# Kernel optimization log

Measured on AMD Instinct MI355X. Metric: run time of the kernel, lower is better.

## Reference

```python
import jax, jax.numpy as jnp
import numpy as np
import math

B, L, D_IN = 4, 8192, 64
H = 256          # d_model
N2 = 32          # d_state // 2 complex conjugate pairs (S4D)
NL = 4           # n_layers
D_OUT = 10


def setup_inputs() -> dict:
    key = jax.random.key(0)
    ks = jax.random.split(key, 16)
    x = jax.random.normal(ks[0], (B, L, D_IN), dtype=jnp.float32)
    # encoder Linear(d_input, d_model)
    enc_W = jax.random.normal(ks[1], (H, D_IN), dtype=jnp.float32) / np.sqrt(D_IN)
    enc_b = jnp.zeros((H,), dtype=jnp.float32)
    # per-layer S4D parameters (stacked over n_layers)
    log_dt = jax.random.uniform(ks[2], (NL, H), dtype=jnp.float32,
                                minval=math.log(1e-3), maxval=math.log(1e-1))
    log_A_re = jnp.full((NL, H, N2), math.log(0.5), dtype=jnp.float32)
    A_im = jnp.tile(math.pi * jnp.arange(N2, dtype=jnp.float32), (NL, H, 1))
    C_re = jax.random.normal(ks[3], (NL, H, N2), dtype=jnp.float32) * (0.5 ** 0.5)
    C_im = jax.random.normal(ks[4], (NL, H, N2), dtype=jnp.float32) * (0.5 ** 0.5)
    D = jax.random.normal(ks[5], (NL, H), dtype=jnp.float32)
    # S4 block output linear (H -> 2H) followed by GLU
    Wo = jax.random.normal(ks[6], (NL, 2 * H, H), dtype=jnp.float32) / np.sqrt(H)
    bo = jnp.zeros((NL, 2 * H), dtype=jnp.float32)
    # post-norm LayerNorm over d_model
    ln_w = jnp.ones((NL, H), dtype=jnp.float32)
    ln_b = jnp.zeros((NL, H), dtype=jnp.float32)
    # final decoder Linear(d_model, d_output)
    out_W = jax.random.normal(ks[7], (D_OUT, H), dtype=jnp.float32) / np.sqrt(H)
    out_b = jnp.zeros((D_OUT,), dtype=jnp.float32)
    return dict(x=x, enc_W=enc_W, enc_b=enc_b, log_dt=log_dt, log_A_re=log_A_re,
                A_im=A_im, C_re=C_re, C_im=C_im, D=D, Wo=Wo, bo=bo,
                ln_w=ln_w, ln_b=ln_b, out_W=out_W, out_b=out_b)


def _s4d_kernel(log_dt, log_A_re, A_im, C_re, C_im, L):
    # S4D-ZOH-ish (S4D-Lin) kernel: K[h,l] = 2 Re sum_n C~[h,n] exp(l*dt*A[h,n])
    dt = jnp.exp(log_dt)[:, None]                      # (H,1)
    A = -jnp.exp(log_A_re) + 1j * A_im                 # (H,N2)
    dtA = dt * A                                       # (H,N2)
    Ct = (C_re + 1j * C_im) * (jnp.exp(dtA) - 1.0) / A # (H,N2)
    t = jnp.arange(L, dtype=jnp.float32)
    V = jnp.exp(dtA[:, :, None] * t)                   # (H,N2,L) Vandermonde
    return 2.0 * jnp.einsum('hn,hnl->hl', Ct, V).real  # (H,L)


def reference(x, enc_W, enc_b, log_dt, log_A_re, A_im, C_re, C_im, D, Wo, bo,
              ln_w, ln_b, out_W, out_b):
    Bc, Lc, _ = x.shape
    h = x @ enc_W.T + enc_b          # (B,L,H)
    h = h.transpose(0, 2, 1)         # (B,H,L) (transposed layout)
    n_layers = log_dt.shape[0]
    for i in range(n_layers):
        K = _s4d_kernel(log_dt[i], log_A_re[i], A_im[i], C_re[i], C_im[i], Lc)
        # FFT convolution (causal, non-circular via 2L padding)
        Kf = jnp.fft.rfft(K, n=2 * Lc)                       # (H, L+1)
        hf = jnp.fft.rfft(h, n=2 * Lc)                       # (B,H,L+1)
        y = jnp.fft.irfft(hf * Kf, n=2 * Lc)[..., :Lc]
        y = y + D[i][:, None] * h                            # skip D*u
        y = jax.nn.gelu(y)
        # output linear (H -> 2H) + GLU, pointwise over length
        u = jnp.einsum('oh,bhl->bol', Wo[i], y) + bo[i][:, None]
        Hd = h.shape[1]
        z = u[:, :Hd] * jax.nn.sigmoid(u[:, Hd:])
        h = z + h                                            # residual
        # post-norm LayerNorm over channel (d_model) dim
        mu = h.mean(axis=1, keepdims=True)
        var = h.var(axis=1, keepdims=True)
        h = (h - mu) / jnp.sqrt(var + 1e-5) * ln_w[i][:, None] + ln_b[i][:, None]
    h = h.transpose(0, 2, 1)          # (B,L,H)
    return h @ out_W.T + out_b        # (B,L,d_output)
```

## Files before the change

### kernel.cpp

```cpp
#include <hip/hip_runtime.h>
#include <hip/hip_bf16.h>


constexpr int B_ = 4, L_ = 8192, DIN = 64, H_ = 256, N2_ = 32, NL_ = 4, DOUT = 10;
constexpr int LC = 64, CHK = L_ / LC;
constexpr int M_ = B_ * L_;

constexpr size_t OFF_EWB  = 1048576;
constexpr size_t OFF_WOB  = 8388608;
constexpr size_t OFF_PWLC = 8781824;
constexpr size_t OFF_UCM  = 8929280;
constexpr size_t OFF_YCM  = 13123584;
constexpr size_t OFF_MTA  = 17317888;
constexpr size_t OFF_MWA  = 19415040;
constexpr size_t OFF_MVA  = 21512192;

typedef short bf16x8 __attribute__((ext_vector_type(8)));
typedef short short8 __attribute__((ext_vector_type(8)));
typedef short short4v __attribute__((ext_vector_type(4)));
typedef float f32x4  __attribute__((ext_vector_type(4)));
typedef int   int2v  __attribute__((ext_vector_type(2)));

__device__ __forceinline__ float b2f(short s) {
    union { float f; unsigned u; } c;
    c.u = ((unsigned)(unsigned short)s) << 16;
    return c.f;
}

__global__ __launch_bounds__(256) void k_wcvt(const float* __restrict__ src,
    __hip_bfloat16* __restrict__ dst, int n4)
{
    int i = blockIdx.x * 256 + threadIdx.x;
    if (i >= n4) return;
    float4 v = ((const float4*)src)[i];
    union { __hip_bfloat16 b[4]; uint2 u; } o;
    o.b[0] = __float2bfloat16(v.x); o.b[1] = __float2bfloat16(v.y);
    o.b[2] = __float2bfloat16(v.z); o.b[3] = __float2bfloat16(v.w);
    ((uint2*)dst)[i] = o.u;
}

__global__ __launch_bounds__(256) void k_mats_all(
    const float* __restrict__ log_dt, const float* __restrict__ log_A_re,
    const float* __restrict__ A_im, const float* __restrict__ C_re,
    const float* __restrict__ C_im, float* __restrict__ ws,
    __hip_bfloat16* __restrict__ mt, __hip_bfloat16* __restrict__ mw,
    __hip_bfloat16* __restrict__ mv)
{
    int bid = blockIdx.x;
    int layer = bid >> 8, h = bid & 255;
    int lh = layer * H_ + h;
    int tid = threadIdx.x;
    __shared__ float zre[32], zim[32], ctr[32], cti[32], kv[64];
    if (tid < 32) {
        int idx = lh * N2_ + tid;
        float dt  = expf(log_dt[lh]);
        float Are = -expf(log_A_re[idx]);
        float Aim = A_im[idx];
        float zr = dt * Are, zi = dt * Aim;
        float er = expf(zr);
        float wre = er * cosf(zi), wim = er * sinf(zi);
        float d = Are * Are + Aim * Aim;
        float nre = wre - 1.f, nim = wim;
        float qre = (nre * Are + nim * Aim) / d;
        float qim = (nim * Are - nre * Aim) / d;
        float cr = C_re[idx], ci = C_im[idx];
        zre[tid] = zr; zim[tid] = zi;
        ctr[tid] = 2.f * (cr * qre - ci * qim);
        cti[tid] = 2.f * (cr * qim + ci * qre);
        float er2 = expf(zr * (float)LC);
        ((float2*)(ws + OFF_PWLC))[idx] =
            make_float2(er2 * cosf(zi * (float)LC), er2 * sinf(zi * (float)LC));
    }
    __syncthreads();
    if (tid < 64) {
        float d = (float)tid, acc = 0.f;
        for (int n = 0; n < 32; n++) {
            float er = expf(zre[n] * d);
            float co = cosf(zim[n] * d), si = sinf(zim[n] * d);
            acc += er * (ctr[n] * co - cti[n] * si);
        }
        kv[tid] = acc;
    }
    __syncthreads();
    {
        int t = tid >> 2, j0 = (tid & 3) * 16;
        alignas(16) __hip_bfloat16 row[16];
        #pragma unroll
        for (int jj = 0; jj < 16; jj++) {
            int j = j0 + jj;
            row[jj] = __float2bfloat16(j <= t ? kv[t - j] : 0.f);
        }
        *(short8*)(mt + (size_t)lh*4096 + t*64 + j0)     = *(short8*)&row[0];
        *(short8*)(mt + (size_t)lh*4096 + t*64 + j0 + 8) = *(short8*)&row[8];
    }
    {
        int n = tid >> 3, j0 = (tid & 7) * 8;
        alignas(16) __hip_bfloat16 rre[8], rim[8];
        #pragma unroll
        for (int jj = 0; jj < 8; jj++) {
            float e = (float)(63 - (j0 + jj));
            float er = expf(zre[n] * e);
            rre[jj] = __float2bfloat16(er * cosf(zim[n] * e));
            rim[jj] = __float2bfloat16(er * sinf(zim[n] * e));
        }
        *(short8*)(mw + (size_t)lh*4096 + (2*n)*64 + j0)   = *(short8*)&rre[0];
        *(short8*)(mw + (size_t)lh*4096 + (2*n+1)*64 + j0) = *(short8*)&rim[0];
    }
    {
        int t = tid >> 2, n0 = (tid & 3) * 8;
        float e = (float)(t + 1);
        alignas(16) __hip_bfloat16 row[16];
        #pragma unroll
        for (int k = 0; k < 8; k++) {
            int n = n0 + k;
            float er = expf(zre[n] * e);
            float wr = er * cosf(zim[n] * e), wi = er * sinf(zim[n] * e);
            row[2*k]   = __float2bfloat16(ctr[n]*wr - cti[n]*wi);
            row[2*k+1] = __float2bfloat16(-(ctr[n]*wi + cti[n]*wr));
        }
        *(short8*)(mv + (size_t)lh*4096 + t*64 + 2*n0)     = *(short8*)&row[0];
        *(short8*)(mv + (size_t)lh*4096 + t*64 + 2*n0 + 8) = *(short8*)&row[8];
    }
}

__global__ __launch_bounds__(256) void k_encoder(const float* __restrict__ x,
    const __hip_bfloat16* __restrict__ ewb, const float* __restrict__ enc_b,
    __hip_bfloat16* __restrict__ u)
{
    __shared__ short sbuf[256 * 66];
    short* xls = sbuf;
    int tid = threadIdx.x;
    int w = tid >> 6, l = tid & 63, l15 = l & 15, l4 = l >> 4;
    int m0 = blockIdx.x * 64;
    int nv = w * 64;
    {
        const float4* x4 = (const float4*)x;
        #pragma unroll
        for (int q = 0; q < 4; q++) {
            int f = tid * 4 + q;
            float4 v = x4[(size_t)m0 * 16 + f];
            int e = f * 4, row = e >> 6, col = e & 63;
            alignas(8) __hip_bfloat16 t4[4] = {
                __float2bfloat16(v.x), __float2bfloat16(v.y),
                __float2bfloat16(v.z), __float2bfloat16(v.w) };
            *(short4v*)&xls[row * 72 + col] = *(short4v*)t4;
        }
    }
    __syncthreads();
    f32x4 acc[4][4];
    #pragma unroll
    for (int mi = 0; mi < 4; mi++)
        #pragma unroll
        for (int nj = 0; nj < 4; nj++) acc[mi][nj] = (f32x4)0.f;
    #pragma unroll
    for (int ks = 0; ks < 2; ks++) {
        int k0 = ks * 32 + l4 * 8;
        bf16x8 a[4];
        #pragma unroll
        for (int mi = 0; mi < 4; mi++)
            a[mi] = *(const bf16x8*)&xls[(mi * 16 + l15) * 72 + k0];
        #pragma unroll
        for (int nj = 0; nj < 4; nj++) {
            bf16x8 b = *(const bf16x8*)(ewb + (size_t)(nv + nj * 16 + l15) * 64 + k0);
            #pragma unroll
            for (int mi = 0; mi < 4; mi++)
                acc[mi][nj] = __builtin_amdgcn_mfma_f32_16x16x32_bf16(a[mi], b, acc[mi][nj], 0, 0, 0);
        }
    }
    float bov[4];
    #pragma unroll
    for (int nj = 0; nj < 4; nj++) bov[nj] = enc_b[nv + nj * 16 + l15];
    __syncthreads();
    #pragma unroll
    for (int mi = 0; mi < 4; mi++)
        #pragma unroll
        for (int r = 0; r < 4; r++) {
            int lr = mi * 16 + l4 * 4 + r;
            #pragma unroll
            for (int nj = 0; nj < 4; nj++) {
                int cn = nv + nj * 16 + l15;
                __hip_bfloat16 bv = __float2bfloat16(acc[mi][nj][r] + bov[nj]);
                sbuf[cn * 66 + lr] = *(short*)&bv;
            }
        }
    __syncthreads();
    #pragma unroll
    for (int q = 0; q < 8; q++)
        *(short8*)(u + (size_t)tid * M_ + m0 + q * 8) = *(short8*)&sbuf[tid * 66 + q * 8];
}

__global__ __launch_bounds__(256) void k_ssm(const __hip_bfloat16* __restrict__ ucm,
    const __hip_bfloat16* __restrict__ mt, const __hip_bfloat16* __restrict__ mw,
    const __hip_bfloat16* __restrict__ mv, const float* __restrict__ ws, int layer,
    const float* __restrict__ Dp, __hip_bfloat16* __restrict__ ycm)
{
    __shared__ __hip_bfloat16 ulds[L_];
    __shared__ __hip_bfloat16 st[CHK * 64];
    __shared__ float segT[8][32][2];
    int h = blockIdx.x >> 2, b = blockIdx.x & 3;
    int tid = threadIdx.x, w = tid >> 6, l = tid & 63, l15 = l & 15, l4 = l >> 4;
    const __hip_bfloat16* ub = ucm + (size_t)h * M_ + (size_t)b * L_;
    #pragma unroll
    for (int it = 0; it < 4; it++) {
        int e0 = it * 2048 + tid * 8;
        short8 v = *(const short8*)(ub + e0);
        int c = e0 >> 6, e = e0 & 63;
        *(short8*)&ulds[c * 64 + (e ^ ((c & 7) << 3))] = v;
    }
    __syncthreads();
    {
        const __hip_bfloat16* bbase = mw + (size_t)h * 4096 + l15 * 64 + l4 * 8;
        #pragma unroll
        for (int half = 0; half < 2; half++) {
            int g0 = (w + half * 4) * 16;
            int ca = g0 + l15;
            f32x4 acc[4];
            #pragma unroll
            for (int nj = 0; nj < 4; nj++) acc[nj] = (f32x4)0.f;
            #pragma unroll
            for (int ks = 0; ks < 2; ks++) {
                int e = l4 * 8 + ks * 32;
                bf16x8 a = *(const bf16x8*)&ulds[ca * 64 + (e ^ ((ca & 7) << 3))];
                #pragma unroll
                for (int nj = 0; nj < 4; nj++) {
                    bf16x8 bb = *(const bf16x8*)(bbase + nj * 16 * 64 + ks * 32);
                    acc[nj] = __builtin_amdgcn_mfma_f32_16x16x32_bf16(a, bb, acc[nj], 0, 0, 0);
                }
            }
            #pragma unroll
            for (int nj = 0; nj < 4; nj++)
                #pragma unroll
                for (int r = 0; r < 4; r++) {
                    int c = g0 + l4 * 4 + r, e = nj * 16 + l15;
                    st[c * 64 + (e ^ ((c & 7) << 3))] = __float2bfloat16(acc[nj][r]);
                }
        }
    }
    __syncthreads();
    {
        int s = tid >> 5, n = tid & 31;
        float2 wl = ((const float2*)(ws + OFF_PWLC))[(size_t)layer * H_ * N2_ + h * 32 + n];
        float tr = 0.f, ti = 0.f;
        for (int j = 0; j < 16; j++) {
            int c = s * 16 + j;
            __hip_bfloat162* p = (__hip_bfloat162*)&st[c * 64 + ((2 * n) ^ ((c & 7) << 3))];
            float2 v = __bfloat1622float2(*p);
            float nr = fmaf(wl.x, tr, v.x); nr = fmaf(-wl.y, ti, nr);
            float ni = fmaf(wl.x, ti, v.y); ni = fmaf(wl.y, tr, ni);
            tr = nr; ti = ni;
        }
        segT[s][n][0] = tr; segT[s][n][1] = ti;
        __syncthreads();
        float wr = wl.x, wi = wl.y;
        #pragma unroll
        for (int q = 0; q < 4; q++) {
            float nr = wr * wr - wi * wi, ni = 2.f * wr * wi;
            wr = nr; wi = ni;
        }
        float ar = 0.f, ai = 0.f;
        for (int t = 0; t < s; t++) {
            float Tx = segT[t][n][0], Ty = segT[t][n][1];
            float nr = fmaf(wr, ar, Tx); nr = fmaf(-wi, ai, nr);
            float ni = fmaf(wr, ai, Ty); ni = fmaf(wi, ar, ni);
            ar = nr; ai = ni;
        }
        for (int j = 0; j < 16; j++) {
            int c = s * 16 + j;
            __hip_bfloat162* p = (__hip_bfloat162*)&st[c * 64 + ((2 * n) ^ ((c & 7) << 3))];
            float2 v = __bfloat1622float2(*p);
            *p = __float22bfloat162_rn(make_float2(ar, ai));
            float nr = fmaf(wl.x, ar, v.x); nr = fmaf(-wl.y, ai, nr);
            float ni = fmaf(wl.x, ai, v.y); ni = fmaf(wl.y, ar, ni);
            ar = nr; ai = ni;
        }
    }
    __syncthreads();
    {
        const __hip_bfloat16* bt = mt + (size_t)h * 4096 + l15 * 64 + l4 * 8;
        const __hip_bfloat16* bv = mv + (size_t)h * 4096 + l15 * 64 + l4 * 8;
        float Dh = Dp[layer * H_ + h];
        __hip_bfloat16* yb = ycm + (size_t)h * M_ + (size_t)b * L_;
        #pragma unroll
        for (int half = 0; half < 2; half++) {
            int g0 = (w + half * 4) * 16;
            int ca = g0 + l15;
            f32x4 acc[4];
            #pragma unroll
            for (int nj = 0; nj < 4; nj++) acc[nj] = (f32x4)0.f;
            #pragma unroll
            for (int ks = 0; ks < 2; ks++) {
                int e = l4 * 8 + ks * 32;
                bf16x8 a = *(const bf16x8*)&ulds[ca * 64 + (e ^ ((ca & 7) << 3))];
                #pragma unroll
                for (int nj = 0; nj < 4; nj++) {
                    bf16x8 bb = *(const bf16x8*)(bt + nj * 16 * 64 + ks * 32);
                    acc[nj] = __builtin_amdgcn_mfma_f32_16x16x32_bf16(a, bb, acc[nj], 0, 0, 0);
                }
            }
            #pragma unroll
            for (int ks = 0; ks < 2; ks++) {
                int e = l4 * 8 + ks * 32;
                bf16x8 a = *(const bf16x8*)&st[ca * 64 + (e ^ ((ca & 7) << 3))];
                #pragma unroll
                for (int nj = 0; nj < 4; nj++) {
                    bf16x8 bb = *(const bf16x8*)(bv + nj * 16 * 64 + ks * 32);
                    acc[nj] = __builtin_amdgcn_mfma_f32_16x16x32_bf16(a, bb, acc[nj], 0, 0, 0);
                }
            }
            #pragma unroll
            for (int nj = 0; nj < 4; nj++)
                #pragma unroll
                for (int r = 0; r < 4; r++) {
                    int g = g0 + l4 * 4 + r;
                    int e = nj * 16 + l15;
                    float uv = __bfloat162float(ulds[g * 64 + (e ^ ((g & 7) << 3))]);
                    float v = fmaf(Dh, uv, acc[nj][r]);
                    float gg = 0.7978845608028654f * fmaf(0.044715f * v, v * v, v);
                    float yv = v / (1.f + __expf(-2.f * gg));
                    yb[(size_t)g * 64 + nj * 16 + l15] = __float2bfloat16(yv);
                }
        }
    }
}

__global__ __launch_bounds__(256) void k_glu_mfma(
    const __hip_bfloat16* __restrict__ ycm,
    const __hip_bfloat16* __restrict__ wob,
    const float* __restrict__ bo, const float* __restrict__ lnw,
    const float* __restrict__ lnb,
    __hip_bfloat16* __restrict__ u)
{
    __shared__ int buf[8320];
    __shared__ float red[4][32][2];
    int* bufA = buf;
    int* bufR = buf + 4160;
    int tid = threadIdx.x;
    int w = tid >> 6, l = tid & 63, l15 = l & 15, l4 = l >> 4;
    int mb = blockIdx.x * 64;
    int nv = w * 64;
    int p = tid & 127, ph = tid >> 7;
    const __hip_bfloat16* aB = ycm + (size_t)(2 * p) * M_ + mb + ph * 16;
    const __hip_bfloat16* rB = u + (size_t)(2 * p) * M_ + mb + ph * 16;

    short8 A0[4], R0[4], A1[4], R1[4];
    A0[0] = *(const short8*)(aB);          A0[1] = *(const short8*)(aB + 8);
    A0[2] = *(const short8*)(aB + M_);     A0[3] = *(const short8*)(aB + M_ + 8);
    R0[0] = *(const short8*)(rB);          R0[1] = *(const short8*)(rB + 8);
    R0[2] = *(const short8*)(rB + M_);     R0[3] = *(const short8*)(rB + M_ + 8);
    A1[0] = *(const short8*)(aB + 32);     A1[1] = *(const short8*)(aB + 40);
    A1[2] = *(const short8*)(aB + M_ + 32);A1[3] = *(const short8*)(aB + M_ + 40);

    float bov[4], bog[4], lw[4], lb[4];
    #pragma unroll
    for (int nj = 0; nj < 4; nj++) {
        int cn = nv + nj * 16 + l15;
        bov[nj] = bo[cn]; bog[nj] = bo[256 + cn];
        lw[nj] = lnw[cn]; lb[nj] = lnb[cn];
    }

    {
        int* da = bufA + ph * 16 * 130 + p;
        int* dr = bufR + ph * 16 * 130 + p;
        #pragma unroll
        for (int j = 0; j < 8; j++) {
            da[j * 130]       = ((int)(unsigned short)A0[0][j]) | (((int)(unsigned short)A0[2][j]) << 16);
            da[(8 + j) * 130] = ((int)(unsigned short)A0[1][j]) | (((int)(unsigned short)A0[3][j]) << 16);
            dr[j * 130]       = ((int)(unsigned short)R0[0][j]) | (((int)(unsigned short)R0[2][j]) << 16);
            dr[(8 + j) * 130] = ((int)(unsigned short)R0[1][j]) | (((int)(unsigned short)R0[3][j]) << 16);
        }
    }
    __syncthreads();

    int abase0 = l15 * 130 + l4 * 4;
    #pragma unroll
    for (int tile = 0; tile < 2; tile++) {
        int m0 = mb + tile * 32;
        f32x4 accv[2][4], accg[2][4];
        #pragma unroll
        for (int sub = 0; sub < 2; sub++)
            #pragma unroll
            for (int nj = 0; nj < 4; nj++) { accv[sub][nj] = (f32x4)0.f; accg[sub][nj] = (f32x4)0.f; }

        #pragma unroll 2
        for (int ks = 0; ks < 8; ks++) {
            int k0 = ks * 32 + l4 * 8;
            union { int2v d[2]; bf16x8 v; } a0u, a1u;
            a0u.d[0] = *(const int2v*)&bufA[abase0 + ks * 16];
            a0u.d[1] = *(const int2v*)&bufA[abase0 + ks * 16 + 2];
            a1u.d[0] = *(const int2v*)&bufA[abase0 + 16 * 130 + ks * 16];
            a1u.d[1] = *(const int2v*)&bufA[abase0 + 16 * 130 + ks * 16 + 2];
            bf16x8 a0 = a0u.v;
            bf16x8 a1 = a1u.v;
            #pragma unroll
            for (int nj = 0; nj < 4; nj++) {
                bf16x8 bv = *(const bf16x8*)(wob + (size_t)(nv + nj * 16 + l15) * H_ + k0);
                bf16x8 bg = *(const bf16x8*)(wob + (size_t)(256 + nv + nj * 16 + l15) * H_ + k0);
                accv[0][nj] = __builtin_amdgcn_mfma_f32_16x16x32_bf16(a0, bv, accv[0][nj], 0, 0, 0);
                accg[0][nj] = __builtin_amdgcn_mfma_f32_16x16x32_bf16(a0, bg, accg[0][nj], 0, 0, 0);
                accv[1][nj] = __builtin_amdgcn_mfma_f32_16x16x32_bf16(a1, bv, accv[1][nj], 0, 0, 0);
                accg[1][nj] = __builtin_amdgcn_mfma_f32_16x16x32_bf16(a1, bg, accg[1][nj], 0, 0, 0);
            }
        }

        const short* bufRs = (const short*)bufR;
        #pragma unroll
        for (int sub = 0; sub < 2; sub++) {
            #pragma unroll
            for (int r = 0; r < 4; r++) {
                int lr = sub * 16 + l4 * 4 + r;
                float s = 0.f, ss = 0.f;
                #pragma unroll
                for (int nj = 0; nj < 4; nj++) {
                    int cn = nv + nj * 16 + l15;
                    float uv = accv[sub][nj][r] + bov[nj];
                    float ug = accg[sub][nj][r] + bog[nj];
                    float z = uv / (1.f + __expf(-ug));
                    float v = z + b2f(bufRs[lr * 260 + cn]);
                    accv[sub][nj][r] = v;
                    s += v; ss += v * v;
                }
                #pragma unroll
                for (int off = 1; off < 16; off <<= 1) {
                    s  += __shfl_xor(s, off);
                    ss += __shfl_xor(ss, off);
                }
                if (l15 == 0) { red[w][lr][0] = s; red[w][lr][1] = ss; }
            }
        }
        if (tile == 0) {
            R1[0] = *(const short8*)(rB + 32);      R1[1] = *(const short8*)(rB + 40);
            R1[2] = *(const short8*)(rB + M_ + 32); R1[3] = *(const short8*)(rB + M_ + 40);
        }
        __syncthreads();
        short* lt = (short*)buf;
        #pragma unroll
        for (int sub = 0; sub < 2; sub++) {
            #pragma unroll
            for (int r = 0; r < 4; r++) {
                int lr = sub * 16 + l4 * 4 + r;
                float s  = red[0][lr][0] + red[1][lr][0] + red[2][lr][0] + red[3][lr][0];
                float ss = red[0][lr][1] + red[1][lr][1] + red[2][lr][1] + red[3][lr][1];
                float mu = s * (1.f / 256.f);
                float var = ss * (1.f / 256.f) - mu * mu;
                float rstd = rsqrtf(var + 1e-5f);
                #pragma unroll
                for (int nj = 0; nj < 4; nj++) {
                    int cn = nv + nj * 16 + l15;
                    float val = (accv[sub][nj][r] - mu) * rstd * lw[nj] + lb[nj];
                    __hip_bfloat16 bval = __float2bfloat16(val);
                    lt[cn * 34 + lr] = *(short*)&bval;
                }
            }
        }
        __syncthreads();
        #pragma unroll
        for (int q = 0; q < 4; q++)
            *(short8*)(u + (size_t)tid * M_ + m0 + q * 8)
                = *(short8*)&lt[tid * 34 + q * 8];
        if (tile == 0) {
            __syncthreads();
            int* da = bufA + ph * 16 * 130 + p;
            int* dr = bufR + ph * 16 * 130 + p;
            #pragma unroll
            for (int j = 0; j < 8; j++) {
                da[j * 130]       = ((int)(unsigned short)A1[0][j]) | (((int)(unsigned short)A1[2][j]) << 16);
                da[(8 + j) * 130] = ((int)(unsigned short)A1[1][j]) | (((int)(unsigned short)A1[3][j]) << 16);
                dr[j * 130]       = ((int)(unsigned short)R1[0][j]) | (((int)(unsigned short)R1[2][j]) << 16);
                dr[(8 + j) * 130] = ((int)(unsigned short)R1[1][j]) | (((int)(unsigned short)R1[3][j]) << 16);
            }
            __syncthreads();
        }
    }
}

__global__ __launch_bounds__(256) void k_decoder(const __hip_bfloat16* __restrict__ u,
    const float* __restrict__ out_W, const float* __restrict__ out_b,
    float* __restrict__ out)
{
    __shared__ int ds[64 * 130];
    __shared__ float wl[10][260];
    int m0 = blockIdx.x * 64;
    int tid = threadIdx.x;
    {
        int p = tid & 127, ph = tid >> 7;
        const __hip_bfloat16* s0 = u + (size_t)(2 * p) * M_ + m0 + ph * 32;
        const __hip_bfloat16* s1 = s0 + M_;
        short8 y0[4], y1[4];
        #pragma unroll
        for (int q = 0; q < 4; q++) {
            y0[q] = *(const short8*)(s0 + q * 8);
            y1[q] = *(const short8*)(s1 + q * 8);
        }
        int* dst = ds + (ph * 32) * 130 + p;
        #pragma unroll
        for (int q = 0; q < 4; q++)
            #pragma unroll
            for (int j = 0; j < 8; j++)
                dst[(q * 8 + j) * 130] =
                    ((int)(unsigned short)y0[q][j]) | (((int)(unsigned short)y1[q][j]) << 16);
    }
    for (int q = tid; q < 640; q += 256) {
        int r = q / 64, k4 = q % 64;
        *(float4*)&wl[r][k4 * 4] = ((const float4*)out_W)[q];
    }
    __syncthreads();
    int slot = tid & 15;
    if (slot < DOUT) {
        #pragma unroll
        for (int pass = 0; pass < 4; pass++) {
            int pl = pass * 16 + (tid >> 4);
            const int* row = ds + pl * 130;
            float a0 = 0.f, a1 = 0.f;
            #pragma unroll 8
            for (int d = 0; d < 128; d++) {
                int v = row[d];
                a0 = fmaf(b2f((short)(v & 0xffff)),  wl[slot][2 * d],     a0);
                a1 = fmaf(b2f((short)(v >> 16)),     wl[slot][2 * d + 1], a1);
            }
            out[(size_t)(m0 + pl) * DOUT + slot] = a0 + a1 + out_b[slot];
        }
    }
}

extern "C" void kernel_launch(void* const* d_in, const int* in_sizes, int n_in,
                              void* d_out, int out_size, void* d_ws, size_t ws_size,
                              hipStream_t stream)
{
    (void)in_sizes; (void)n_in; (void)out_size; (void)ws_size;
    const float* x        = (const float*)d_in[0];
    const float* enc_W    = (const float*)d_in[1];
    const float* enc_b    = (const float*)d_in[2];
    const float* log_dt   = (const float*)d_in[3];
    const float* log_A_re = (const float*)d_in[4];
    const float* A_im     = (const float*)d_in[5];
    const float* C_re     = (const float*)d_in[6];
    const float* C_im     = (const float*)d_in[7];
    const float* Dp       = (const float*)d_in[8];
    const float* Wo       = (const float*)d_in[9];
    const float* bo       = (const float*)d_in[10];
    const float* lnw      = (const float*)d_in[11];
    const float* lnb      = (const float*)d_in[12];
    const float* out_W    = (const float*)d_in[13];
    const float* out_b    = (const float*)d_in[14];
    float* ws = (float*)d_ws;
    __hip_bfloat16* ewb = (__hip_bfloat16*)(ws + OFF_EWB);
    __hip_bfloat16* u   = (__hip_bfloat16*)(ws + OFF_UCM);
    __hip_bfloat16* ycm = (__hip_bfloat16*)(ws + OFF_YCM);
    __hip_bfloat16* mtA = (__hip_bfloat16*)(ws + OFF_MTA);
    __hip_bfloat16* mwA = (__hip_bfloat16*)(ws + OFF_MWA);
    __hip_bfloat16* mvA = (__hip_bfloat16*)(ws + OFF_MVA);
    __hip_bfloat16* wob = (__hip_bfloat16*)(ws + OFF_WOB);

    k_wcvt<<<(NL_ * 2 * H_ * H_ / 4 + 255) / 256, 256, 0, stream>>>(Wo, wob, NL_ * 2 * H_ * H_ / 4);
    k_wcvt<<<(H_ * DIN / 4 + 255) / 256, 256, 0, stream>>>(enc_W, ewb, H_ * DIN / 4);
    k_mats_all<<<NL_ * H_, 256, 0, stream>>>(log_dt, log_A_re, A_im, C_re, C_im,
                                             ws, mtA, mwA, mvA);
    k_encoder<<<M_ / 64, 256, 0, stream>>>(x, ewb, enc_b, u);
    for (int i = 0; i < NL_; i++) {
        k_ssm<<<H_ * B_, 256, 0, stream>>>(u,
            mtA + (size_t)i * H_ * 4096, mwA + (size_t)i * H_ * 4096,
            mvA + (size_t)i * H_ * 4096, ws, i, Dp, ycm);
        k_glu_mfma<<<M_ / 64, 256, 0, stream>>>(ycm,
            wob + (size_t)i * 2 * H_ * H_, bo + (size_t)i * 2 * H_,
            lnw + (size_t)i * H_, lnb + (size_t)i * H_, u);
    }
    k_decoder<<<M_ / 64, 256, 0, stream>>>(u, out_W, out_b, (float*)d_out);
}
```

Baseline: 362.1 us.

## Process both GLU row tiles concurrently with 512-thread blocks, merge weight conversions

The GLU+LayerNorm kernel now runs with 512 threads per block. Each half of the block handles one 32-row tile at the same time, where before a 256-thread block walked the two tiles in sequence. All A and residual loads are issued up front. The residual is staged into shared memory after the MFMA phase, and the final transpose buffer covers all 64 rows. The two weight conversion launches are merged into one kernel. This adds parallelism and cuts serialized syncs per block, at the cost of higher register and LDS pressure per block and possibly lower occupancy.

```diff
diff --git a/kernel.cpp b/kernel.cpp
--- a/kernel.cpp
+++ b/kernel.cpp
@@ -27,16 +27,20 @@
     return c.f;
 }
 
-__global__ __launch_bounds__(256) void k_wcvt(const float* __restrict__ src,
-    __hip_bfloat16* __restrict__ dst, int n4)
+__global__ __launch_bounds__(256) void k_wcvt2(const float* __restrict__ a,
+    __hip_bfloat16* __restrict__ da, int n4a, const float* __restrict__ b,
+    __hip_bfloat16* __restrict__ db, int n4b)
 {
     int i = blockIdx.x * 256 + threadIdx.x;
-    if (i >= n4) return;
-    float4 v = ((const float4*)src)[i];
-    union { __hip_bfloat16 b[4]; uint2 u; } o;
-    o.b[0] = __float2bfloat16(v.x); o.b[1] = __float2bfloat16(v.y);
-    o.b[2] = __float2bfloat16(v.z); o.b[3] = __float2bfloat16(v.w);
-    ((uint2*)dst)[i] = o.u;
+    const float* s; __hip_bfloat16* d; int j;
+    if (i < n4a) { s = a; d = da; j = i; }
+    else if (i < n4a + n4b) { s = b; d = db; j = i - n4a; }
+    else return;
+    float4 v = ((const float4*)s)[j];
+    union { __hip_bfloat16 bb[4]; uint2 u; } o;
+    o.bb[0] = __float2bfloat16(v.x); o.bb[1] = __float2bfloat16(v.y);
+    o.bb[2] = __float2bfloat16(v.z); o.bb[3] = __float2bfloat16(v.w);
+    ((uint2*)d)[j] = o.u;
 }
 
 __global__ __launch_bounds__(256) void k_mats_all(
@@ -47,8 +51,7 @@
     __hip_bfloat16* __restrict__ mv)
 {
     int bid = blockIdx.x;
-    int layer = bid >> 8, h = bid & 255;
-    int lh = layer * H_ + h;
+    int lh = bid;
     int tid = threadIdx.x;
     __shared__ float zre[32], zim[32], ctr[32], cti[32], kv[64];
     if (tid < 32) {
@@ -323,32 +326,33 @@
     }
 }
 
-__global__ __launch_bounds__(256) void k_glu_mfma(
+__global__ __launch_bounds__(512) void k_glu_mfma(
     const __hip_bfloat16* __restrict__ ycm,
     const __hip_bfloat16* __restrict__ wob,
     const float* __restrict__ bo, const float* __restrict__ lnw,
     const float* __restrict__ lnb,
     __hip_bfloat16* __restrict__ u)
 {
-    __shared__ int buf[8320];
-    __shared__ float red[4][32][2];
-    int* bufA = buf;
-    int* bufR = buf + 4160;
+    __shared__ int buf[8704];
+    __shared__ float red[2][4][32][2];
     int tid = threadIdx.x;
-    int w = tid >> 6, l = tid & 63, l15 = l & 15, l4 = l >> 4;
+    int wt = tid >> 8;
+    int t2 = tid & 255;
+    int w = t2 >> 6, l = t2 & 63, l15 = l & 15, l4 = l >> 4;
     int mb = blockIdx.x * 64;
     int nv = w * 64;
-    int p = tid & 127, ph = tid >> 7;
-    const __hip_bfloat16* aB = ycm + (size_t)(2 * p) * M_ + mb + ph * 16;
-    const __hip_bfloat16* rB = u + (size_t)(2 * p) * M_ + mb + ph * 16;
-
-    short8 A0[4], R0[4], A1[4], R1[4];
-    A0[0] = *(const short8*)(aB);          A0[1] = *(const short8*)(aB + 8);
-    A0[2] = *(const short8*)(aB + M_);     A0[3] = *(const short8*)(aB + M_ + 8);
-    R0[0] = *(const short8*)(rB);          R0[1] = *(const short8*)(rB + 8);
-    R0[2] = *(const short8*)(rB + M_);     R0[3] = *(const short8*)(rB + M_ + 8);
-    A1[0] = *(const short8*)(aB + 32);     A1[1] = *(const short8*)(aB + 40);
-    A1[2] = *(const short8*)(aB + M_ + 32);A1[3] = *(const short8*)(aB + M_ + 40);
+    int p = tid & 127, q2 = tid >> 7;
+
+    const __hip_bfloat16* aB = ycm + (size_t)(2 * p) * M_ + mb + q2 * 16;
+    const __hip_bfloat16* rB = u + (size_t)(2 * p) * M_ + mb + q2 * 16;
+    short8 A0a = *(const short8*)(aB);
+    short8 A0b = *(const short8*)(aB + 8);
+    short8 A1a = *(const short8*)(aB + M_);
+    short8 A1b = *(const short8*)(aB + M_ + 8);
+    short8 R0a = *(const short8*)(rB);
+    short8 R0b = *(const short8*)(rB + 8);
+    short8 R1a = *(const short8*)(rB + M_);
+    short8 R1b = *(const short8*)(rB + M_ + 8);
 
     float bov[4], bog[4], lw[4], lb[4];
     #pragma unroll
@@ -359,116 +363,113 @@
     }
 
     {
-        int* da = bufA + ph * 16 * 130 + p;
-        int* dr = bufR + ph * 16 * 130 + p;
+        int* da = buf + q2 * 16 * 130 + p;
         #pragma unroll
         for (int j = 0; j < 8; j++) {
-            da[j * 130]       = ((int)(unsigned short)A0[0][j]) | (((int)(unsigned short)A0[2][j]) << 16);
-            da[(8 + j) * 130] = ((int)(unsigned short)A0[1][j]) | (((int)(unsigned short)A0[3][j]) << 16);
-            dr[j * 130]       = ((int)(unsigned short)R0[0][j]) | (((int)(unsigned short)R0[2][j]) << 16);
-            dr[(8 + j) * 130] = ((int)(unsigned short)R0[1][j]) | (((int)(unsigned short)R0[3][j]) << 16);
-        }
-    }
-    __syncthreads();
-
-    int abase0 = l15 * 130 + l4 * 4;
-    #pragma unroll
-    for (int tile = 0; tile < 2; tile++) {
-        int m0 = mb + tile * 32;
-        f32x4 accv[2][4], accg[2][4];
-        #pragma unroll
-        for (int sub = 0; sub < 2; sub++)
-            #pragma unroll
-            for (int nj = 0; nj < 4; nj++) { accv[sub][nj] = (f32x4)0.f; accg[sub][nj] = (f32x4)0.f; }
-
-        #pragma unroll 2
-        for (int ks = 0; ks < 8; ks++) {
-            int k0 = ks * 32 + l4 * 8;
-            union { int2v d[2]; bf16x8 v; } a0u, a1u;
-            a0u.d[0] = *(const int2v*)&bufA[abase0 + ks * 16];
-            a0u.d[1] = *(const int2v*)&bufA[abase0 + ks * 16 + 2];
-            a1u.d[0] = *(const int2v*)&bufA[abase0 + 16 * 130 + ks * 16];
-            a1u.d[1] = *(const int2v*)&bufA[abase0 + 16 * 130 + ks * 16 + 2];
-            bf16x8 a0 = a0u.v;
-            bf16x8 a1 = a1u.v;
+            da[j * 130]       = ((int)(unsigned short)A0a[j]) | (((int)(unsigned short)A1a[j]) << 16);
+            da[(8 + j) * 130] = ((int)(unsigned short)A0b[j]) | (((int)(unsigned short)A1b[j]) << 16);
+        }
+    }
+    __syncthreads();
+
+    f32x4 accv[2][4], accg[2][4];
+    #pragma unroll
+    for (int sub = 0; sub < 2; sub++)
+        #pragma unroll
+        for (int nj = 0; nj < 4; nj++) { accv[sub][nj] = (f32x4)0.f; accg[sub][nj] = (f32x4)0.f; }
+
+    int abase0 = (wt * 32 + l15) * 130 + l4 * 4;
+    #pragma unroll 2
+    for (int ks = 0; ks < 8; ks++) {
+        int k0 = ks * 32 + l4 * 8;
+        union { int2v d[2]; bf16x8 v; } a0u, a1u;
+        a0u.d[0] = *(const int2v*)&buf[abase0 + ks * 16];
+        a0u.d[1] = *(const int2v*)&buf[abase0 + ks * 16 + 2];
+        a1u.d[0] = *(const int2v*)&buf[abase0 + 16 * 130 + ks * 16];
+        a1u.d[1] = *(const int2v*)&buf[abase0 + 16 * 130 + ks * 16 + 2];
+        bf16x8 a0 = a0u.v;
+        bf16x8 a1 = a1u.v;
+        #pragma unroll
+        for (int nj = 0; nj < 4; nj++) {
+            bf16x8 bv = *(const bf16x8*)(wob + (size_t)(nv + nj * 16 + l15) * H_ + k0);
+            bf16x8 bg = *(const bf16x8*)(wob + (size_t)(256 + nv + nj * 16 + l15) * H_ + k0);
+            accv[0][nj] = __builtin_amdgcn_mfma_f32_16x16x32_bf16(a0, bv, accv[0][nj], 0, 0, 0);
+            accg[0][nj] = __builtin_amdgcn_mfma_f32_16x16x32_bf16(a0, bg, accg[0][nj], 0, 0, 0);
+            accv[1][nj] = __builtin_amdgcn_mfma_f32_16x16x32_bf16(a1, bv, accv[1][nj], 0, 0, 0);
+            accg[1][nj] = __builtin_amdgcn_mfma_f32_16x16x32_bf16(a1, bg, accg[1][nj], 0, 0, 0);
+        }
+    }
+    __syncthreads();
+
+    {
+        int* dr = buf + q2 * 16 * 130 + p;
+        #pragma unroll
+        for (int j = 0; j < 8; j++) {
+            dr[j * 130]       = ((int)(unsigned short)R0a[j]) | (((int)(unsigned short)R1a[j]) << 16);
+            dr[(8 + j) * 130] = ((int)(unsigned short)R0b[j]) | (((int)(unsigned short)R1b[j]) << 16);
+        }
+    }
+    __syncthreads();
+
+    const short* bufRs = (const short*)buf;
+    #pragma unroll
+    for (int sub = 0; sub < 2; sub++) {
+        #pragma unroll
+        for (int r = 0; r < 4; r++) {
+            int lr = sub * 16 + l4 * 4 + r;
+            int gr = wt * 32 + lr;
+            float s = 0.f, ss = 0.f;
             #pragma unroll
             for (int nj = 0; nj < 4; nj++) {
-                bf16x8 bv = *(const bf16x8*)(wob + (size_t)(nv + nj * 16 + l15) * H_ + k0);
-                bf16x8 bg = *(const bf16x8*)(wob + (size_t)(256 + nv + nj * 16 + l15) * H_ + k0);
-                accv[0][nj] = __builtin_amdgcn_mfma_f32_16x16x32_bf16(a0, bv, accv[0][nj], 0, 0, 0);
-                accg[0][nj] = __builtin_amdgcn_mfma_f32_16x16x32_bf16(a0, bg, accg[0][nj], 0, 0, 0);
-                accv[1][nj] = __builtin_amdgcn_mfma_f32_16x16x32_bf16(a1, bv, accv[1][nj], 0, 0, 0);
-                accg[1][nj] = __builtin_amdgcn_mfma_f32_16x16x32_bf16(a1, bg, accg[1][nj], 0, 0, 0);
-            }
-        }
-
-        const short* bufRs = (const short*)bufR;
-        #pragma unroll
-        for (int sub = 0; sub < 2; sub++) {
-            #pragma unroll
-            for (int r = 0; r < 4; r++) {
-                int lr = sub * 16 + l4 * 4 + r;
-                float s = 0.f, ss = 0.f;
-                #pragma unroll
-                for (int nj = 0; nj < 4; nj++) {
-                    int cn = nv + nj * 16 + l15;
-                    float uv = accv[sub][nj][r] + bov[nj];
-                    float ug = accg[sub][nj][r] + bog[nj];
-                    float z = uv / (1.f + __expf(-ug));
-                    float v = z + b2f(bufRs[lr * 260 + cn]);
-                    accv[sub][nj][r] = v;
-                    s += v; ss += v * v;
-                }
-                #pragma unroll
-                for (int off = 1; off < 16; off <<= 1) {
-                    s  += __shfl_xor(s, off);
-                    ss += __shfl_xor(ss, off);
-                }
-                if (l15 == 0) { red[w][lr][0] = s; red[w][lr][1] = ss; }
-            }
-        }
-        if (tile == 0) {
-            R1[0] = *(const short8*)(rB + 32);      R1[1] = *(const short8*)(rB + 40);
-            R1[2] = *(const short8*)(rB + M_ + 32); R1[3] = *(const short8*)(rB + M_ + 40);
-        }
-        __syncthreads();
-        short* lt = (short*)buf;
-        #pragma unroll
-        for (int sub = 0; sub < 2; sub++) {
-            #pragma unroll
-            for (int r = 0; r < 4; r++) {
-                int lr = sub * 16 + l4 * 4 + r;
-                float s  = red[0][lr][0] + red[1][lr][0] + red[2][lr][0] + red[3][lr][0];
-                float ss = red[0][lr][1] + red[1][lr][1] + red[2][lr][1] + red[3][lr][1];
-                float mu = s * (1.f / 256.f);
-                float var = ss * (1.f / 256.f) - mu * mu;
-                float rstd = rsqrtf(var + 1e-5f);
-                #pragma unroll
-                for (int nj = 0; nj < 4; nj++) {
-                    int cn = nv + nj * 16 + l15;
-                    float val = (accv[sub][nj][r] - mu) * rstd * lw[nj] + lb[nj];
-                    __hip_bfloat16 bval = __float2bfloat16(val);
-                    lt[cn * 34 + lr] = *(short*)&bval;
-                }
-            }
-        }
-        __syncthreads();
-        #pragma unroll
-        for (int q = 0; q < 4; q++)
-            *(short8*)(u + (size_t)tid * M_ + m0 + q * 8)
-                = *(short8*)&lt[tid * 34 + q * 8];
-        if (tile == 0) {
-            __syncthreads();
-            int* da = bufA + ph * 16 * 130 + p;
-            int* dr = bufR + ph * 16 * 130 + p;
-            #pragma unroll
-            for (int j = 0; j < 8; j++) {
-                da[j * 130]       = ((int)(unsigned short)A1[0][j]) | (((int)(unsigned short)A1[2][j]) << 16);
-                da[(8 + j) * 130] = ((int)(unsigned short)A1[1][j]) | (((int)(unsigned short)A1[3][j]) << 16);
-                dr[j * 130]       = ((int)(unsigned short)R1[0][j]) | (((int)(unsigned short)R1[2][j]) << 16);
-                dr[(8 + j) * 130] = ((int)(unsigned short)R1[1][j]) | (((int)(unsigned short)R1[3][j]) << 16);
-            }
-            __syncthreads();
+                int cn = nv + nj * 16 + l15;
+                float uv = accv[sub][nj][r] + bov[nj];
+                float ug = accg[sub][nj][r] + bog[nj];
+                float z = uv / (1.f + __expf(-ug));
+                float v = z + b2f(bufRs[gr * 260 + cn]);
+                accv[sub][nj][r] = v;
+                s += v; ss += v * v;
+            }
+            #pragma unroll
+            for (int off = 1; off < 16; off <<= 1) {
+                s  += __shfl_xor(s, off);
+                ss += __shfl_xor(ss, off);
+            }
+            if (l15 == 0) { red[wt][w][lr][0] = s; red[wt][w][lr][1] = ss; }
+        }
+    }
+    __syncthreads();
+    short* lt = (short*)buf;
+    #pragma unroll
+    for (int sub = 0; sub < 2; sub++) {
+        #pragma unroll
+        for (int r = 0; r < 4; r++) {
+            int lr = sub * 16 + l4 * 4 + r;
+            int gr = wt * 32 + lr;
+            float s  = red[wt][0][lr][0] + red[wt][1][lr][0] + red[wt][2][lr][0] + red[wt][3][lr][0];
+            float ss = red[wt][0][lr][1] + red[wt][1][lr][1] + red[wt][2][lr][1] + red[wt][3][lr][1];
+            float mu = s * (1.f / 256.f);
+            float var = ss * (1.f / 256.f) - mu * mu;
+            float rstd = rsqrtf(var + 1e-5f);
+            #pragma unroll
+            for (int nj = 0; nj < 4; nj++) {
+                int cn = nv + nj * 16 + l15;
+                float val = (accv[sub][nj][r] - mu) * rstd * lw[nj] + lb[nj];
+                __hip_bfloat16 bval = __float2bfloat16(val);
+                lt[cn * 68 + gr] = *(short*)&bval;
+            }
+        }
+    }
+    __syncthreads();
+    {
+        int ch = tid >> 1, hf = tid & 1;
+        const short4v* lp = (const short4v*)(lt + ch * 68 + hf * 32);
+        __hip_bfloat16* up = u + (size_t)ch * M_ + mb + hf * 32;
+        #pragma unroll
+        for (int q = 0; q < 4; q++) {
+            alignas(16) short tmp8[8];
+            *(short4v*)&tmp8[0] = lp[q * 2];
+            *(short4v*)&tmp8[4] = lp[q * 2 + 1];
+            *(short8*)(up + q * 8) = *(short8*)tmp8;
         }
     }
 }
@@ -551,8 +552,8 @@
     __hip_bfloat16* mvA = (__hip_bfloat16*)(ws + OFF_MVA);
     __hip_bfloat16* wob = (__hip_bfloat16*)(ws + OFF_WOB);
 
-    k_wcvt<<<(NL_ * 2 * H_ * H_ / 4 + 255) / 256, 256, 0, stream>>>(Wo, wob, NL_ * 2 * H_ * H_ / 4);
-    k_wcvt<<<(H_ * DIN / 4 + 255) / 256, 256, 0, stream>>>(enc_W, ewb, H_ * DIN / 4);
+    int n4a = NL_ * 2 * H_ * H_ / 4, n4b = H_ * DIN / 4;
+    k_wcvt2<<<(n4a + n4b + 255) / 256, 256, 0, stream>>>(Wo, wob, n4a, enc_W, ewb, n4b);
     k_mats_all<<<NL_ * H_, 256, 0, stream>>>(log_dt, log_A_re, A_im, C_re, C_im,
                                              ws, mtA, mwA, mvA);
     k_encoder<<<M_ / 64, 256, 0, stream>>>(x, ewb, enc_b, u);
@@ -560,7 +561,7 @@
         k_ssm<<<H_ * B_, 256, 0, stream>>>(u,
             mtA + (size_t)i * H_ * 4096, mwA + (size_t)i * H_ * 4096,
             mvA + (size_t)i * H_ * 4096, ws, i, Dp, ycm);
-        k_glu_mfma<<<M_ / 64, 256, 0, stream>>>(ycm,
+        k_glu_mfma<<<M_ / 64, 512, 0, stream>>>(ycm,
             wob + (size_t)i * 2 * H_ * H_, bo + (size_t)i * 2 * H_,
             lnw + (size_t)i * H_, lnb + (size_t)i * H_, u);
     }
```

New measurement: 386.1 us. 6.6% more time.
